# Optimization experiments

Hardware: AMD Instinct MI355X
Metric: run time of the kernel (lower is better)

The kernel has to match this reference:

```python
import jax, jax.numpy as jnp
import numpy as np
from jax.ops import segment_sum, segment_max

DIM = 64; EDGE_DIM = 6; ACTION_DIM = 6
N = 16384; E = 32768; G = 256; TPG = 12  # nodes, edges, graphs, torsions/graph


def setup_inputs() -> dict:
    key = jax.random.key(0)
    ks = jax.random.split(key, 16)
    d = DIM
    def lin(k, fo, fi):
        return (jax.random.normal(k, (fo, fi), jnp.float32) / np.sqrt(fi)).astype(jnp.float32)
    return {
        "x": jax.random.normal(ks[0], (N, 3), jnp.float32),
        "edge_attr": jax.random.normal(ks[1], (E, EDGE_DIM), jnp.float32),
        "edge_index": jax.random.randint(ks[2], (2, E), 0, N),
        "batch": (jnp.arange(N) // (N // G)).astype(jnp.int32),
        "nonring": jax.random.randint(ks[3], (G * TPG, 4), 0, N),
        "nrbidx": (jnp.arange(G * TPG) // TPG).astype(jnp.int32),
        "num_graphs": G,
        "torsion_size": TPG,
        "lin0_w": lin(ks[4], d, 3), "lin0_b": jnp.zeros((d,), jnp.float32),
        "e1_w": lin(ks[5], d, EDGE_DIM), "e1_b": jnp.zeros((d,), jnp.float32),
        "e2_w": lin(ks[6], d * d, d), "e2_b": jnp.zeros((d * d,), jnp.float32),
        "root_w": lin(ks[7], d, d), "conv_b": jnp.zeros((d,), jnp.float32),
        "gru_wih": lin(ks[8], 3 * d, d), "gru_whh": lin(ks[9], 3 * d, d),
        "gru_bih": jnp.zeros((3 * d,), jnp.float32), "gru_bhh": jnp.zeros((3 * d,), jnp.float32),
        "s2s_wih": lin(ks[10], 4 * d, 2 * d), "s2s_whh": lin(ks[11], 4 * d, d),
        "s2s_bih": jnp.zeros((4 * d,), jnp.float32), "s2s_bhh": jnp.zeros((4 * d,), jnp.float32),
        "mem_wih": lin(ks[12], 4 * d, 2 * d), "mem_whh": lin(ks[13], 4 * d, d),
        "mem_bih": jnp.zeros((4 * d,), jnp.float32), "mem_bhh": jnp.zeros((4 * d,), jnp.float32),
        "lin1_w": lin(ks[14], d, 5 * d), "lin1_b": jnp.zeros((d,), jnp.float32),
        "lin2_w": lin(ks[15], ACTION_DIM, d), "lin2_b": jnp.zeros((ACTION_DIM,), jnp.float32),
    }


def _lstm_step(xin, h, c, wih, whh, bih, bhh):
    g = xin @ wih.T + bih + h @ whh.T + bhh
    i, f, gg, o = jnp.split(g, 4, axis=-1)
    c = jax.nn.sigmoid(f) * c + jax.nn.sigmoid(i) * jnp.tanh(gg)
    h = jax.nn.sigmoid(o) * jnp.tanh(c)
    return h, c


def _model(x, edge_attr, lin0_w, lin0_b, e1_w, e1_b, e2_w, e2_b, root_w, conv_b,
           gru_wih, gru_whh, gru_bih, gru_bhh, s2s_wih, s2s_whh, s2s_bih, s2s_bhh,
           mem_wih, mem_whh, mem_bih, mem_bhh, lin1_w, lin1_b, lin2_w, lin2_b,
           edge_index, batch, nonring, nrbidx, num_graphs, torsion_size):
    d = lin0_w.shape[0]
    n = x.shape[0]
    out = jax.nn.relu(x @ lin0_w.T + lin0_b)           # [N, d]
    h = out                                            # GRU hidden
    src, dst = edge_index[0], edge_index[1]
    # edge-conditioned weights (fixed across the 6 iterations -> computed once)
    ew = (jax.nn.relu(edge_attr @ e1_w.T + e1_b) @ e2_w.T + e2_b).reshape(-1, d, d)  # [E, d, d]
    deg = jnp.clip(segment_sum(jnp.ones((src.shape[0],), out.dtype), dst, num_segments=n), 1.0)
    for _ in range(6):
        msg = jnp.einsum('ei,eio->eo', out[src], ew)   # per-edge matmul, [E, d]
        agg = segment_sum(msg, dst, num_segments=n) / deg[:, None]  # scatter-mean
        m = jax.nn.relu(agg + out @ root_w + conv_b)
        gi = m @ gru_wih.T + gru_bih
        gh = h @ gru_whh.T + gru_bhh
        r = jax.nn.sigmoid(gi[:, :d] + gh[:, :d])
        z = jax.nn.sigmoid(gi[:, d:2 * d] + gh[:, d:2 * d])
        nnew = jnp.tanh(gi[:, 2 * d:] + r * gh[:, 2 * d:])
        h = (1.0 - z) * nnew + z * h
        out = h
    # Set2Set pooling, 6 processing steps
    q_star = jnp.zeros((num_graphs, 2 * d), out.dtype)
    hs = jnp.zeros((num_graphs, d), out.dtype); cs = jnp.zeros_like(hs)
    for _ in range(6):
        hs, cs = _lstm_step(q_star, hs, cs, s2s_wih, s2s_whh, s2s_bih, s2s_bhh)
        e = jnp.sum(out * hs[batch], axis=-1)
        emax = segment_max(e, batch, num_segments=num_graphs)
        a = jnp.exp(e - emax[batch])
        a = a / segment_sum(a, batch, num_segments=num_graphs)[batch]
        r_ = segment_sum(a[:, None] * out, batch, num_segments=num_graphs)
        q_star = jnp.concatenate([hs, r_], axis=-1)
    # memory LSTM, single step from zero state
    hx = jnp.zeros((num_graphs, d), out.dtype); cx = jnp.zeros_like(hx)
    hx, cx = _lstm_step(q_star, hx, cx, mem_wih, mem_whh, mem_bih, mem_bhh)
    lstm_sel = hx[nrbidx]                                   # [T, d]
    node_sel = out[nonring.reshape(-1)].reshape(4, -1, d)   # faithful to .view(4,-1,dim)
    stacked = jnp.concatenate([lstm_sel[None], node_sel], axis=0)  # [5, T, d]
    feat = jnp.transpose(stacked, (2, 1, 0)).reshape(-1, 5 * d)    # faithful permute+reshape -> [T, 5d]
    o1 = jax.nn.relu(feat @ lin1_w.T + lin1_b)
    logits = o1 @ lin2_w.T + lin2_b                          # [T, action_dim]
    logit = logits.reshape(num_graphs, torsion_size, -1)     # uniform split + pad_sequence
    return logit, hx[None], cx[None]


def reference(x, edge_attr, edge_index, batch, nonring, nrbidx, num_graphs, torsion_size,
              lin0_w, lin0_b, e1_w, e1_b, e2_w, e2_b, root_w, conv_b,
              gru_wih, gru_whh, gru_bih, gru_bhh, s2s_wih, s2s_whh, s2s_bih, s2s_bhh,
              mem_wih, mem_whh, mem_bih, mem_bhh, lin1_w, lin1_b, lin2_w, lin2_b):
    return _model(x, edge_attr, lin0_w, lin0_b, e1_w, e1_b, e2_w, e2_b, root_w, conv_b,
                  gru_wih, gru_whh, gru_bih, gru_bhh, s2s_wih, s2s_whh, s2s_bih, s2s_bhh,
                  mem_wih, mem_whh, mem_bih, mem_bhh, lin1_w, lin1_b, lin2_w, lin2_b,
                  edge_index, batch, nonring, nrbidx, num_graphs, torsion_size)
```

## Files before the change

### kernel.cpp

```cpp
#include <hip/hip_runtime.h>

#define NNODE 16384
#define NEDGE 32768
#define NG    256
#define TPGx  12
#define TTOT  (NG * TPGx)
#define D     64

typedef _Float16 h8 __attribute__((ext_vector_type(8)));
typedef _Float16 h4 __attribute__((ext_vector_type(4)));
typedef float    f4 __attribute__((ext_vector_type(4)));

static __device__ __forceinline__ float sigm(float x) { return 1.f / (1.f + __expf(-x)); }
static __device__ __forceinline__ float tanh_f(float x) {
  float t = __expf(2.f * x);
  return (t - 1.f) / (t + 1.f);
}

static __device__ __forceinline__ f4 mfma16h(h8 a, h8 b, f4 c) {
  return __builtin_amdgcn_mfma_f32_16x16x32_f16(a, b, c, 0, 0, 0);
}

static __device__ __forceinline__ h8 splat16(_Float16 x) {
  h8 v = {x, x, x, x, x, x, x, x};
  return v;
}

#define WS_H      0
#define WS_AGG    4194304
#define WS_W2     8388608
#define WS_RT     8921088
#define WS_WHH    8929280
#define WS_WIH    8953856
#define WS_SWIHT  8978432
#define WS_SWHHT  9109504
#define WS_MWIHT  9175040
#define WS_L1WT   9306112
#define WS_L2WF   9388032
#define WS_FB     9389568
#define WS_DEG    9398784
#define WS_HX     9464320
#define WS_NEED   9529856

struct Srcs { const void* p[23]; };

__device__ __constant__ const int kCum[24] = {
    0, 192, 256, 640, 704, 262848, 266944, 271040, 271104, 283392, 295680,
    295872, 296064, 328832, 345216, 345472, 345728, 378496, 378752, 379008,
    399488, 399552, 399936, 399942};

__global__ __launch_bounds__(256) void setup1_kernel(Srcs S, char* __restrict__ ws) {
  int idx = blockIdx.x * 256 + threadIdx.x;
  if (idx < 399942) {
    int r = 0, base = 0;
#pragma unroll
    for (int k = 0; k < 23; k++)
      if (idx >= kCum[k]) { r = k; base = kCum[k]; }
    int li = idx - base;
    float v = ((const float*)S.p[r])[li];

    float*    fb    = (float*)(ws + WS_FB);
    _Float16* w2    = (_Float16*)(ws + WS_W2);
    _Float16* rtH   = (_Float16*)(ws + WS_RT);
    _Float16* whhH  = (_Float16*)(ws + WS_WHH);
    _Float16* wihH  = (_Float16*)(ws + WS_WIH);
    float*    swihT = (float*)(ws + WS_SWIHT);
    float*    swhhT = (float*)(ws + WS_SWHHT);
    float*    mwihT = (float*)(ws + WS_MWIHT);
    float*    l1wT  = (float*)(ws + WS_L1WT);
    float*    l2w   = (float*)(ws + WS_L2WF);

    switch (r) {
      case 0: fb[li] = v; break;
      case 1: fb[192 + li] = v; break;
      case 2: fb[256 + li] = v; break;
      case 3: fb[640 + li] = v; break;
      case 4: {
        int i = li >> 12, o = (li >> 6) & 63, k = li & 63;
        w2[i * 4096 + (((k >> 3) * 64 + o) << 3) + (k & 7)] = (_Float16)v;
      } break;
      case 5: {
        int k = li >> 6, o = li & 63;
        w2[64 * 4096 + (((k >> 3) * 64 + o) << 3) + (k & 7)] = (_Float16)v;
      } break;
      case 6: {
        int i = li >> 6, o = li & 63;
        rtH[o * 64 + i] = (_Float16)v;
      } break;
      case 7: fb[704 + li] = v; break;
      case 8: wihH[li] = (_Float16)v; break;
      case 9: whhH[li] = (_Float16)v; break;
      case 10: fb[768 + li] = v; break;
      case 11: fb[960 + li] = v; break;
      case 12: swihT[(li & 127) * 256 + (li >> 7)] = v; break;
      case 13: swhhT[(li & 63) * 256 + (li >> 6)] = v; break;
      case 14: fb[1152 + li] = v; break;
      case 15: fb[1408 + li] = v; break;
      case 16: mwihT[(li & 127) * 256 + (li >> 7)] = v; break;
      case 17: fb[1664 + li] = v; break;
      case 18: fb[1920 + li] = v; break;
      case 19: l1wT[(li % 320) * 64 + (li / 320)] = v; break;
      case 20: fb[2176 + li] = v; break;
      case 21: l2w[li] = v; break;
      case 22: fb[2240 + li] = v; break;
    }
    return;
  }
  idx -= 399942;
  float4 z4 = {0.f, 0.f, 0.f, 0.f};
  if (idx < 262144) { ((float4*)(ws + WS_AGG))[idx] = z4; return; }
  idx -= 262144;
  if (idx < 4096) ((float4*)(ws + WS_DEG))[idx] = z4;
}
#define SETUP1_N (399942 + 262144 + 4096)

__global__ __launch_bounds__(256) void setup2_kernel(
    const float* __restrict__ x, const int* __restrict__ edge_index,
    char* __restrict__ ws) {
  int idx = blockIdx.x * 256 + threadIdx.x;
  if (idx < 262144) {
    const float* fb = (const float*)(ws + WS_FB);
    float* h = (float*)(ws + WS_H);
    int n = idx >> 4, oq = idx & 15;
    float x0 = x[n * 3], x1 = x[n * 3 + 1], x2 = x[n * 3 + 2];
    float4 out;
#pragma unroll
    for (int c = 0; c < 4; c++) {
      int o = oq * 4 + c;
      float acc = fb[192 + o] + x0 * fb[o * 3] + x1 * fb[o * 3 + 1] + x2 * fb[o * 3 + 2];
      ((float*)&out)[c] = fmaxf(acc, 0.f);
    }
    *(float4*)&h[n * 64 + oq * 4] = out;
    return;
  }
  idx -= 262144;
  if (idx < NEDGE) {
    float* deg = (float*)(ws + WS_DEG);
    atomicAdd(&deg[edge_index[NEDGE + idx]], 1.0f);
  }
}
#define SETUP2_N (262144 + NEDGE)

__global__ __launch_bounds__(256) void msg_kernel(
    const float* __restrict__ h, const float* __restrict__ ea,
    const float* __restrict__ fb, const _Float16* __restrict__ w2,
    const int* __restrict__ edge_index, float* __restrict__ agg) {
  __shared__ _Float16 sOut[64][72];
  const int tid = threadIdx.x;
  const int wave = tid >> 6, lane = tid & 63;
  const int m15 = lane & 15, quad = lane >> 4;
  const int eb = blockIdx.x * 64;
  {
    int r = tid >> 2, c0 = (tid & 3) * 16;
    int srcn = edge_index[eb + r];
#pragma unroll
    for (int c = c0; c < c0 + 16; c += 4) {
      float4 v = *(const float4*)&h[srcn * D + c];
      sOut[r][c]     = (_Float16)v.x;
      sOut[r][c + 1] = (_Float16)v.y;
      sOut[r][c + 2] = (_Float16)v.z;
      sOut[r][c + 3] = (_Float16)v.w;
    }
  }
  h8 hid0[4], hid1[4];
#pragma unroll
  for (int r = 0; r < 4; r++) {
    int e = eb + r * 16 + m15;
    float eav[6];
#pragma unroll
    for (int j = 0; j < 6; j++) eav[j] = ea[e * 6 + j];
#pragma unroll
    for (int j = 0; j < 8; j++) {
      int k0 = quad * 8 + j, k1 = 32 + quad * 8 + j;
      float a0 = fb[640 + k0], a1 = fb[640 + k1];
#pragma unroll
      for (int jj = 0; jj < 6; jj++) {
        a0 += eav[jj] * fb[256 + k0 * 6 + jj];
        a1 += eav[jj] * fb[256 + k1 * 6 + jj];
      }
      hid0[r][j] = (_Float16)fmaxf(a0, 0.f);
      hid1[r][j] = (_Float16)fmaxf(a1, 0.f);
    }
  }
  __syncthreads();
  const _Float16* bp0 = w2 + (quad * 64 + wave * 16 + m15) * 8;
  const _Float16* bp1 = w2 + ((4 + quad) * 64 + wave * 16 + m15) * 8;
  f4 zz = {0.f, 0.f, 0.f, 0.f};
  f4 acc[4];
#pragma unroll
  for (int r = 0; r < 4; r++) acc[r] = zz;
  h8 c0[4], c1[4];
#pragma unroll
  for (int t = 0; t < 4; t++) {
    c0[t] = *(const h8*)(bp0 + t * 4096);
    c1[t] = *(const h8*)(bp1 + t * 4096);
  }
#pragma unroll
  for (int p = 0; p < 16; p++) {
    h8 n0[4], n1[4];
    if (p < 15) {
#pragma unroll
      for (int t = 0; t < 4; t++) {
        int i = (p + 1) * 4 + t;
        n0[t] = *(const h8*)(bp0 + i * 4096);
        n1[t] = *(const h8*)(bp1 + i * 4096);
      }
    }
#pragma unroll
    for (int r = 0; r < 4; r++) {
      h4 os4 = *(const h4*)&sOut[r * 16 + m15][p * 4];
#pragma unroll
      for (int t = 0; t < 4; t++) {
        h8 os = splat16(os4[t]);
        acc[r] = mfma16h(hid0[r] * os, c0[t], acc[r]);
        acc[r] = mfma16h(hid1[r] * os, c1[t], acc[r]);
      }
    }
    if (p < 15) {
#pragma unroll
      for (int t = 0; t < 4; t++) { c0[t] = n0[t]; c1[t] = n1[t]; }
    }
  }
  {
    h8 b0 = *(const h8*)(bp0 + 64 * 4096);
    h8 b1 = *(const h8*)(bp1 + 64 * 4096);
#pragma unroll
    for (int r = 0; r < 4; r++) {
      h8 a0 = *(const h8*)&sOut[r * 16 + m15][quad * 8];
      h8 a1 = *(const h8*)&sOut[r * 16 + m15][32 + quad * 8];
      acc[r] = mfma16h(a0, b0, acc[r]);
      acc[r] = mfma16h(a1, b1, acc[r]);
    }
  }
#pragma unroll
  for (int r = 0; r < 4; r++) {
#pragma unroll
    for (int reg = 0; reg < 4; reg++) {
      int ee = eb + r * 16 + quad * 4 + reg;
      int dn = edge_index[NEDGE + ee];
      atomicAdd(agg + dn * D + wave * 16 + m15, acc[r][reg]);
    }
  }
}

__global__ __launch_bounds__(64) void update_kernel(
    float* __restrict__ h, float* __restrict__ agg, const float* __restrict__ deg,
    const _Float16* __restrict__ rtH, const _Float16* __restrict__ whhH,
    const _Float16* __restrict__ wihH, const float* __restrict__ fb) {
  __shared__ float bufH[16][68];
  __shared__ float bufM[16][68];
  const int lane = threadIdx.x;
  const int m15 = lane & 15, quad = lane >> 4;
  const int nb = blockIdx.x * 16;
  {
    int r = lane >> 2, c0 = (lane & 3) * 16;
#pragma unroll
    for (int c = c0; c < c0 + 16; c += 4)
      *(float4*)&bufH[r][c] = *(const float4*)&h[(nb + r) * D + c];
  }
  __syncthreads();
  h8 a0, a1;
#pragma unroll
  for (int j = 0; j < 8; j++) {
    a0[j] = (_Float16)bufH[m15][quad * 8 + j];
    a1[j] = (_Float16)bufH[m15][32 + quad * 8 + j];
  }
  f4 zz = {0.f, 0.f, 0.f, 0.f};
  f4 acc[16];
#pragma unroll
  for (int nt = 0; nt < 16; nt++) acc[nt] = zz;
#pragma unroll
  for (int nt = 0; nt < 16; nt++) {
    int nn = nt * 16 + m15;
    const _Float16* bp = (nt < 4) ? (rtH + nn * D) : (whhH + (nn - 64) * D);
    h8 bh0 = *(const h8*)(bp + quad * 8);
    h8 bh1 = *(const h8*)(bp + 32 + quad * 8);
    f4 a = acc[nt];
    a = mfma16h(a0, bh0, a);
    a = mfma16h(a1, bh1, a);
    acc[nt] = a;
  }
#pragma unroll
  for (int nt = 0; nt < 4; nt++) {
#pragma unroll
    for (int reg = 0; reg < 4; reg++) {
      int nloc = quad * 4 + reg;
      int o = nt * 16 + m15;
      float dg = fmaxf(deg[nb + nloc], 1.f);
      int aidx = (nb + nloc) * D + o;
      float v = acc[nt][reg] + agg[aidx] / dg + fb[704 + o];
      agg[aidx] = 0.f;
      bufM[nloc][o] = fmaxf(v, 0.f);
    }
  }
  __syncthreads();
  h8 m0, m1;
#pragma unroll
  for (int j = 0; j < 8; j++) {
    m0[j] = (_Float16)bufM[m15][quad * 8 + j];
    m1[j] = (_Float16)bufM[m15][32 + quad * 8 + j];
  }
  f4 g2[12];
#pragma unroll
  for (int nt = 0; nt < 12; nt++) g2[nt] = zz;
#pragma unroll
  for (int nt = 0; nt < 12; nt++) {
    int nn = nt * 16 + m15;
    const _Float16* bp = wihH + nn * D;
    h8 bh0 = *(const h8*)(bp + quad * 8);
    h8 bh1 = *(const h8*)(bp + 32 + quad * 8);
    f4 a = g2[nt];
    a = mfma16h(m0, bh0, a);
    a = mfma16h(m1, bh1, a);
    g2[nt] = a;
  }
#pragma unroll
  for (int nt = 0; nt < 4; nt++) {
#pragma unroll
    for (int reg = 0; reg < 4; reg++) {
      int nloc = quad * 4 + reg;
      int o = nt * 16 + m15;
      int gidx = (nb + nloc) * D + o;
      float gir = g2[nt][reg]      + fb[768 + o];
      float giz = g2[nt + 4][reg]  + fb[768 + 64 + o];
      float gin = g2[nt + 8][reg]  + fb[768 + 128 + o];
      float ghr = acc[nt + 4][reg]  + fb[960 + o];
      float ghz = acc[nt + 8][reg]  + fb[960 + 64 + o];
      float ghn = acc[nt + 12][reg] + fb[960 + 128 + o];
      float rr = sigm(gir + ghr);
      float zg = sigm(giz + ghz);
      float nnv = tanh_f(gin + rr * ghn);
      float hv = h[gidx];
      h[gidx] = (1.f - zg) * nnv + zg * hv;
    }
  }
}

__global__ __launch_bounds__(256) void s2s_kernel(
    const float* __restrict__ h,
    const float* __restrict__ wihT, const float* __restrict__ whhT,
    const float* __restrict__ mwihT, const float* __restrict__ fb,
    float* __restrict__ hx_f32, float* __restrict__ dout) {
  __shared__ float outL[64][65];
  __shared__ float qs[128];
  __shared__ float hsv[64], csv[64], sg[256], sa[64];
  const int t = threadIdx.x;
  const int g = blockIdx.x;
  float wr[128];
#pragma unroll
  for (int j = 0; j < 128; j++) wr[j] = wihT[j * 256 + t];
  for (int idx = t; idx < 64 * 64; idx += 256) outL[idx >> 6][idx & 63] = h[g * 4096 + idx];
  if (t < 128) qs[t] = 0.f;
  if (t < 64) { hsv[t] = 0.f; csv[t] = 0.f; }
  __syncthreads();
  for (int step = 0; step < 6; step++) {
    float acc = fb[1152 + t] + fb[1408 + t];
#pragma unroll
    for (int j = 0; j < 128; j++) acc += qs[j] * wr[j];
#pragma unroll 8
    for (int j = 0; j < 64; j++) acc += hsv[j] * whhT[j * 256 + t];
    sg[t] = acc;
    __syncthreads();
    if (t < 64) {
      float cn = sigm(sg[64 + t]) * csv[t] + sigm(sg[t]) * tanh_f(sg[128 + t]);
      csv[t] = cn;
      float hv = sigm(sg[192 + t]) * tanh_f(cn);
      hsv[t] = hv;
      float e = 0.f;
      for (int d2 = 0; d2 < 64; d2++) e += outL[t][d2] * hsv[d2];
      float mx = e;
      for (int off = 32; off > 0; off >>= 1) mx = fmaxf(mx, __shfl_xor(mx, off));
      float a = __expf(e - mx);
      float s = a;
      for (int off = 32; off > 0; off >>= 1) s += __shfl_xor(s, off);
      sa[t] = a / s;
      float r = 0.f;
      for (int n2 = 0; n2 < 64; n2++) r += sa[n2] * outL[n2][t];
      qs[t] = hv;
      qs[64 + t] = r;
    }
    __syncthreads();
  }
  float acc = fb[1664 + t] + fb[1920 + t];
#pragma unroll 8
  for (int j = 0; j < 128; j++) acc += qs[j] * mwihT[j * 256 + t];
  sg[t] = acc;
  __syncthreads();
  if (t < 64) {
    float cn = sigm(sg[t]) * tanh_f(sg[128 + t]);
    float hn = sigm(sg[192 + t]) * tanh_f(cn);
    hx_f32[g * 64 + t] = hn;
    dout[TTOT * 6 + g * 64 + t] = hn;
    dout[TTOT * 6 + NG * 64 + g * 64 + t] = cn;
  }
}

__global__ __launch_bounds__(64) void head_kernel(
    const float* __restrict__ h, const float* __restrict__ hx_f32,
    const int* __restrict__ nonring, const int* __restrict__ nrbidx,
    const float* __restrict__ l1wT, const float* __restrict__ l2w,
    const float* __restrict__ fb, float* __restrict__ dout) {
  __shared__ float feat[320];
  __shared__ float so1[64];
  const int r = blockIdx.x;
  const int lane = threadIdx.x;
  const int blk = r % 48, di = r / 48;
  const int tt = blk * 64 + lane;
  feat[lane * 5] = hx_f32[nrbidx[tt] * 64 + di];
#pragma unroll
  for (int s = 1; s <= 4; s++)
    feat[lane * 5 + s] = h[nonring[(s - 1) * TTOT + tt] * 64 + di];
  __syncthreads();
  float acc = fb[2176 + lane];
#pragma unroll 8
  for (int c = 0; c < 320; c++) acc += feat[c] * l1wT[c * 64 + lane];
  so1[lane] = fmaxf(acc, 0.f);
  __syncthreads();
  if (lane < 6) {
    float a2 = fb[2240 + lane];
    for (int j = 0; j < 64; j++) a2 += so1[j] * l2w[lane * 64 + j];
    dout[r * 6 + lane] = a2;
  }
}

extern "C" void kernel_launch(void* const* d_in, const int* in_sizes, int n_in,
                              void* d_out, int out_size, void* d_ws, size_t ws_size,
                              hipStream_t stream) {
  (void)in_sizes; (void)n_in; (void)out_size;
  const float* x         = (const float*)d_in[0];
  const float* edge_attr = (const float*)d_in[1];
  const int* edge_index  = (const int*)d_in[2];
  const int* nonring     = (const int*)d_in[4];
  const int* nrbidx      = (const int*)d_in[5];
  float* out = (float*)d_out;

  char* ws = (char*)d_ws;
  float*    h      = (float*)(ws + WS_H);
  float*    agg    = (float*)(ws + WS_AGG);
  _Float16* w2     = (_Float16*)(ws + WS_W2);
  _Float16* rtH    = (_Float16*)(ws + WS_RT);
  _Float16* whhH   = (_Float16*)(ws + WS_WHH);
  _Float16* wihH   = (_Float16*)(ws + WS_WIH);
  float*    swihT  = (float*)(ws + WS_SWIHT);
  float*    swhhT  = (float*)(ws + WS_SWHHT);
  float*    mwihT  = (float*)(ws + WS_MWIHT);
  float*    l1wT   = (float*)(ws + WS_L1WT);
  float*    l2wF   = (float*)(ws + WS_L2WF);
  float*    fb     = (float*)(ws + WS_FB);
  float*    deg    = (float*)(ws + WS_DEG);
  float*    hx_f32 = (float*)(ws + WS_HX);
  if (ws_size < (size_t)WS_NEED) return;

  Srcs S;
  S.p[0] = d_in[8];   S.p[1] = d_in[9];   S.p[2] = d_in[10];  S.p[3] = d_in[11];
  S.p[4] = d_in[12];  S.p[5] = d_in[13];  S.p[6] = d_in[14];  S.p[7] = d_in[15];
  S.p[8] = d_in[16];  S.p[9] = d_in[17];  S.p[10] = d_in[18]; S.p[11] = d_in[19];
  S.p[12] = d_in[20]; S.p[13] = d_in[21]; S.p[14] = d_in[22]; S.p[15] = d_in[23];
  S.p[16] = d_in[24]; S.p[17] = d_in[26]; S.p[18] = d_in[27]; S.p[19] = d_in[28];
  S.p[20] = d_in[29]; S.p[21] = d_in[30]; S.p[22] = d_in[31];

  setup1_kernel<<<(SETUP1_N + 255) / 256, 256, 0, stream>>>(S, ws);
  setup2_kernel<<<(SETUP2_N + 255) / 256, 256, 0, stream>>>(x, edge_index, ws);

  for (int it = 0; it < 6; it++) {
    msg_kernel<<<NEDGE / 64, 256, 0, stream>>>(h, edge_attr, fb, w2, edge_index, agg);
    update_kernel<<<NNODE / 16, 64, 0, stream>>>(h, agg, deg, rtH, whhH, wihH, fb);
  }

  s2s_kernel<<<NG, 256, 0, stream>>>(h, swihT, swhhT, mwihT, fb, hx_f32, out);
  head_kernel<<<TTOT, 64, 0, stream>>>(h, hx_f32, nonring, nrbidx, l1wT, l2wF, fb, out);
}
```

Measured before the change: 444.5 us.

## Replace atomic scatter aggregation with CSR gather of per-edge messages

Edge messages are now written to a dense per-edge buffer, and a CSR index of incoming edges per destination node is built once at setup. The update kernel sums each node's messages by gathering through that index, so the float atomics and the per-iteration zeroing of the aggregation buffer go away. Update blocks now handle 8 nodes instead of 16, which doubles the grid but leaves half of each MFMA tile idle. The cost is an extra 8 MB message buffer write and read per iteration, plus two small setup kernels, one of which is a single-block serial prefix scan.

```diff
diff --git a/kernel.cpp b/kernel.cpp
--- a/kernel.cpp
+++ b/kernel.cpp
@@ -27,20 +27,23 @@
 }
 
 #define WS_H      0
-#define WS_AGG    4194304
-#define WS_W2     8388608
-#define WS_RT     8921088
-#define WS_WHH    8929280
-#define WS_WIH    8953856
-#define WS_SWIHT  8978432
-#define WS_SWHHT  9109504
-#define WS_MWIHT  9175040
-#define WS_L1WT   9306112
-#define WS_L2WF   9388032
-#define WS_FB     9389568
-#define WS_DEG    9398784
-#define WS_HX     9464320
-#define WS_NEED   9529856
+#define WS_MSG    4194304
+#define WS_W2     12582912
+#define WS_RT     13115392
+#define WS_WHH    13123584
+#define WS_WIH    13148160
+#define WS_SWIHT  13172736
+#define WS_SWHHT  13303808
+#define WS_MWIHT  13369344
+#define WS_L1WT   13500416
+#define WS_L2WF   13582336
+#define WS_FB     13583872
+#define WS_DEG    13592896
+#define WS_CSROFF 13658432
+#define WS_CURS   13723984
+#define WS_CSRE   13789520
+#define WS_HX     13920592
+#define WS_NEED   13986304
 
 struct Srcs { const void* p[23]; };
 
@@ -108,11 +111,9 @@
   }
   idx -= 399942;
   float4 z4 = {0.f, 0.f, 0.f, 0.f};
-  if (idx < 262144) { ((float4*)(ws + WS_AGG))[idx] = z4; return; }
-  idx -= 262144;
   if (idx < 4096) ((float4*)(ws + WS_DEG))[idx] = z4;
 }
-#define SETUP1_N (399942 + 262144 + 4096)
+#define SETUP1_N (399942 + 4096)
 
 __global__ __launch_bounds__(256) void setup2_kernel(
     const float* __restrict__ x, const int* __restrict__ edge_index,
@@ -141,10 +142,47 @@
 }
 #define SETUP2_N (262144 + NEDGE)
 
+__global__ __launch_bounds__(256) void setup3_kernel(char* __restrict__ ws) {
+  __shared__ int part[256];
+  const float* deg = (const float*)(ws + WS_DEG);
+  int* csroff = (int*)(ws + WS_CSROFF);
+  int* curs   = (int*)(ws + WS_CURS);
+  const int t = threadIdx.x;
+  int s = 0;
+  for (int j = 0; j < 64; j++) s += (int)deg[t * 64 + j];
+  part[t] = s;
+  __syncthreads();
+  if (t == 0) {
+    int run = 0;
+    for (int k = 0; k < 256; k++) { int v = part[k]; part[k] = run; run += v; }
+  }
+  __syncthreads();
+  int off = part[t];
+  for (int j = 0; j < 64; j++) {
+    int n = t * 64 + j;
+    csroff[n] = off;
+    off += (int)deg[n];
+    curs[n] = 0;
+  }
+  if (t == 255) csroff[NNODE] = NEDGE;
+}
+
+__global__ __launch_bounds__(256) void setup4_kernel(const int* __restrict__ edge_index,
+                                                     char* __restrict__ ws) {
+  int e = blockIdx.x * 256 + threadIdx.x;
+  if (e >= NEDGE) return;
+  const int* csroff = (const int*)(ws + WS_CSROFF);
+  int* curs = (int*)(ws + WS_CURS);
+  int* csre = (int*)(ws + WS_CSRE);
+  int dst = edge_index[NEDGE + e];
+  int pos = atomicAdd(&curs[dst], 1);
+  csre[csroff[dst] + pos] = e;
+}
+
 __global__ __launch_bounds__(256) void msg_kernel(
     const float* __restrict__ h, const float* __restrict__ ea,
     const float* __restrict__ fb, const _Float16* __restrict__ w2,
-    const int* __restrict__ edge_index, float* __restrict__ agg) {
+    const int* __restrict__ edge_index, float* __restrict__ msgbuf) {
   __shared__ _Float16 sOut[64][72];
   const int tid = threadIdx.x;
   const int wave = tid >> 6, lane = tid & 63;
@@ -237,33 +275,53 @@
 #pragma unroll
     for (int reg = 0; reg < 4; reg++) {
       int ee = eb + r * 16 + quad * 4 + reg;
-      int dn = edge_index[NEDGE + ee];
-      atomicAdd(agg + dn * D + wave * 16 + m15, acc[r][reg]);
+      msgbuf[ee * D + wave * 16 + m15] = acc[r][reg];
     }
   }
 }
 
 __global__ __launch_bounds__(64) void update_kernel(
-    float* __restrict__ h, float* __restrict__ agg, const float* __restrict__ deg,
+    float* __restrict__ h, const float* __restrict__ msgbuf,
+    const float* __restrict__ deg, const int* __restrict__ csroff,
+    const int* __restrict__ csre,
     const _Float16* __restrict__ rtH, const _Float16* __restrict__ whhH,
     const _Float16* __restrict__ wihH, const float* __restrict__ fb) {
-  __shared__ float bufH[16][68];
-  __shared__ float bufM[16][68];
+  __shared__ float bufH[8][68];
+  __shared__ float bufM[8][68];
   const int lane = threadIdx.x;
   const int m15 = lane & 15, quad = lane >> 4;
-  const int nb = blockIdx.x * 16;
+  const int m7 = m15 & 7;
+  const int nb = blockIdx.x * 8;
   {
-    int r = lane >> 2, c0 = (lane & 3) * 16;
-#pragma unroll
-    for (int c = c0; c < c0 + 16; c += 4)
+    int r = lane >> 3, c0 = (lane & 7) * 8;
+#pragma unroll
+    for (int c = c0; c < c0 + 8; c += 4)
       *(float4*)&bufH[r][c] = *(const float4*)&h[(nb + r) * D + c];
   }
   __syncthreads();
+  float aggv[4][4];
+#pragma unroll
+  for (int reg = 0; reg < 4; reg++)
+#pragma unroll
+    for (int nt = 0; nt < 4; nt++) aggv[reg][nt] = 0.f;
+#pragma unroll
+  for (int reg = 0; reg < 4; reg++) {
+    int nloc = quad * 4 + reg;
+    if (nloc < 8) {
+      int n = nb + nloc;
+      int be = csroff[n], en = csroff[n + 1];
+      for (int e2 = be; e2 < en; e2++) {
+        const float* mp = msgbuf + csre[e2] * D + m15;
+#pragma unroll
+        for (int nt = 0; nt < 4; nt++) aggv[reg][nt] += mp[nt * 16];
+      }
+    }
+  }
   h8 a0, a1;
 #pragma unroll
   for (int j = 0; j < 8; j++) {
-    a0[j] = (_Float16)bufH[m15][quad * 8 + j];
-    a1[j] = (_Float16)bufH[m15][32 + quad * 8 + j];
+    a0[j] = (_Float16)bufH[m7][quad * 8 + j];
+    a1[j] = (_Float16)bufH[m7][32 + quad * 8 + j];
   }
   f4 zz = {0.f, 0.f, 0.f, 0.f};
   f4 acc[16];
@@ -285,20 +343,20 @@
 #pragma unroll
     for (int reg = 0; reg < 4; reg++) {
       int nloc = quad * 4 + reg;
-      int o = nt * 16 + m15;
-      float dg = fmaxf(deg[nb + nloc], 1.f);
-      int aidx = (nb + nloc) * D + o;
-      float v = acc[nt][reg] + agg[aidx] / dg + fb[704 + o];
-      agg[aidx] = 0.f;
-      bufM[nloc][o] = fmaxf(v, 0.f);
+      if (nloc < 8) {
+        int o = nt * 16 + m15;
+        float dg = fmaxf(deg[nb + nloc], 1.f);
+        float v = acc[nt][reg] + aggv[reg][nt] / dg + fb[704 + o];
+        bufM[nloc][o] = fmaxf(v, 0.f);
+      }
     }
   }
   __syncthreads();
   h8 m0, m1;
 #pragma unroll
   for (int j = 0; j < 8; j++) {
-    m0[j] = (_Float16)bufM[m15][quad * 8 + j];
-    m1[j] = (_Float16)bufM[m15][32 + quad * 8 + j];
+    m0[j] = (_Float16)bufM[m7][quad * 8 + j];
+    m1[j] = (_Float16)bufM[m7][32 + quad * 8 + j];
   }
   f4 g2[12];
 #pragma unroll
@@ -319,19 +377,21 @@
 #pragma unroll
     for (int reg = 0; reg < 4; reg++) {
       int nloc = quad * 4 + reg;
-      int o = nt * 16 + m15;
-      int gidx = (nb + nloc) * D + o;
-      float gir = g2[nt][reg]      + fb[768 + o];
-      float giz = g2[nt + 4][reg]  + fb[768 + 64 + o];
-      float gin = g2[nt + 8][reg]  + fb[768 + 128 + o];
-      float ghr = acc[nt + 4][reg]  + fb[960 + o];
-      float ghz = acc[nt + 8][reg]  + fb[960 + 64 + o];
-      float ghn = acc[nt + 12][reg] + fb[960 + 128 + o];
-      float rr = sigm(gir + ghr);
-      float zg = sigm(giz + ghz);
-      float nnv = tanh_f(gin + rr * ghn);
-      float hv = h[gidx];
-      h[gidx] = (1.f - zg) * nnv + zg * hv;
+      if (nloc < 8) {
+        int o = nt * 16 + m15;
+        int gidx = (nb + nloc) * D + o;
+        float gir = g2[nt][reg]      + fb[768 + o];
+        float giz = g2[nt + 4][reg]  + fb[768 + 64 + o];
+        float gin = g2[nt + 8][reg]  + fb[768 + 128 + o];
+        float ghr = acc[nt + 4][reg]  + fb[960 + o];
+        float ghz = acc[nt + 8][reg]  + fb[960 + 64 + o];
+        float ghn = acc[nt + 12][reg] + fb[960 + 128 + o];
+        float rr = sigm(gir + ghr);
+        float zg = sigm(giz + ghz);
+        float nnv = tanh_f(gin + rr * ghn);
+        float hv = h[gidx];
+        h[gidx] = (1.f - zg) * nnv + zg * hv;
+      }
     }
   }
 }
@@ -436,7 +496,7 @@
 
   char* ws = (char*)d_ws;
   float*    h      = (float*)(ws + WS_H);
-  float*    agg    = (float*)(ws + WS_AGG);
+  float*    msgbuf = (float*)(ws + WS_MSG);
   _Float16* w2     = (_Float16*)(ws + WS_W2);
   _Float16* rtH    = (_Float16*)(ws + WS_RT);
   _Float16* whhH   = (_Float16*)(ws + WS_WHH);
@@ -448,6 +508,8 @@
   float*    l2wF   = (float*)(ws + WS_L2WF);
   float*    fb     = (float*)(ws + WS_FB);
   float*    deg    = (float*)(ws + WS_DEG);
+  int*      csroff = (int*)(ws + WS_CSROFF);
+  int*      csre   = (int*)(ws + WS_CSRE);
   float*    hx_f32 = (float*)(ws + WS_HX);
   if (ws_size < (size_t)WS_NEED) return;
 
@@ -461,10 +523,13 @@
 
   setup1_kernel<<<(SETUP1_N + 255) / 256, 256, 0, stream>>>(S, ws);
   setup2_kernel<<<(SETUP2_N + 255) / 256, 256, 0, stream>>>(x, edge_index, ws);
+  setup3_kernel<<<1, 256, 0, stream>>>(ws);
+  setup4_kernel<<<NEDGE / 256, 256, 0, stream>>>(edge_index, ws);
 
   for (int it = 0; it < 6; it++) {
-    msg_kernel<<<NEDGE / 64, 256, 0, stream>>>(h, edge_attr, fb, w2, edge_index, agg);
-    update_kernel<<<NNODE / 16, 64, 0, stream>>>(h, agg, deg, rtH, whhH, wihH, fb);
+    msg_kernel<<<NEDGE / 64, 256, 0, stream>>>(h, edge_attr, fb, w2, edge_index, msgbuf);
+    update_kernel<<<NNODE / 8, 64, 0, stream>>>(h, msgbuf, deg, csroff, csre,
+                                                rtH, whhH, wihH, fb);
   }
 
   s2s_kernel<<<NG, 256, 0, stream>>>(h, swihT, swhhT, mwihT, fb, hx_f32, out);
```

Result: slower. 513.0 us (+15.4%).

## Split message kernel K-dimension across two wave halves with shared-memory reduction

Applied to the files above, without the earlier changes.

The message kernel now launches 512 threads per block, with two groups of four waves each handling half of the 64 input-feature chunks of the edge-conditioned weight product. The second half adds the root term and writes its partial accumulators to shared memory. After a barrier the first half sums the partials and performs the atomic scatter. This halves the serial MFMA chain per wave to raise parallelism and latency hiding, at the cost of extra LDS use, a second barrier and duplicated edge-hidden computation in each half.

```diff
diff --git a/kernel.cpp b/kernel.cpp
--- a/kernel.cpp
+++ b/kernel.cpp
@@ -141,20 +141,23 @@
 }
 #define SETUP2_N (262144 + NEDGE)
 
-__global__ __launch_bounds__(256) void msg_kernel(
+__global__ __launch_bounds__(512, 4) void msg_kernel(
     const float* __restrict__ h, const float* __restrict__ ea,
     const float* __restrict__ fb, const _Float16* __restrict__ w2,
     const int* __restrict__ edge_index, float* __restrict__ agg) {
   __shared__ _Float16 sOut[64][72];
+  __shared__ float part[4][64][17];
   const int tid = threadIdx.x;
   const int wave = tid >> 6, lane = tid & 63;
   const int m15 = lane & 15, quad = lane >> 4;
+  const int w4 = wave & 3;
+  const int half = wave >> 2;
   const int eb = blockIdx.x * 64;
   {
-    int r = tid >> 2, c0 = (tid & 3) * 16;
+    int r = tid >> 3, c0 = (tid & 7) * 8;
     int srcn = edge_index[eb + r];
 #pragma unroll
-    for (int c = c0; c < c0 + 16; c += 4) {
+    for (int c = c0; c < c0 + 8; c += 4) {
       float4 v = *(const float4*)&h[srcn * D + c];
       sOut[r][c]     = (_Float16)v.x;
       sOut[r][c + 1] = (_Float16)v.y;
@@ -183,62 +186,74 @@
     }
   }
   __syncthreads();
-  const _Float16* bp0 = w2 + (quad * 64 + wave * 16 + m15) * 8;
-  const _Float16* bp1 = w2 + ((4 + quad) * 64 + wave * 16 + m15) * 8;
+  const _Float16* bp0 = w2 + (quad * 64 + w4 * 16 + m15) * 8;
+  const _Float16* bp1 = w2 + ((4 + quad) * 64 + w4 * 16 + m15) * 8;
+  const int tbase = half * 32;
   f4 zz = {0.f, 0.f, 0.f, 0.f};
   f4 acc[4];
 #pragma unroll
   for (int r = 0; r < 4; r++) acc[r] = zz;
-  h8 c0[4], c1[4];
+  h8 c0v[4], c1v[4];
 #pragma unroll
   for (int t = 0; t < 4; t++) {
-    c0[t] = *(const h8*)(bp0 + t * 4096);
-    c1[t] = *(const h8*)(bp1 + t * 4096);
-  }
-#pragma unroll
-  for (int p = 0; p < 16; p++) {
+    c0v[t] = *(const h8*)(bp0 + (tbase + t) * 4096);
+    c1v[t] = *(const h8*)(bp1 + (tbase + t) * 4096);
+  }
+#pragma unroll
+  for (int p = 0; p < 8; p++) {
     h8 n0[4], n1[4];
-    if (p < 15) {
+    if (p < 7) {
 #pragma unroll
       for (int t = 0; t < 4; t++) {
-        int i = (p + 1) * 4 + t;
+        int i = tbase + (p + 1) * 4 + t;
         n0[t] = *(const h8*)(bp0 + i * 4096);
         n1[t] = *(const h8*)(bp1 + i * 4096);
       }
     }
 #pragma unroll
     for (int r = 0; r < 4; r++) {
-      h4 os4 = *(const h4*)&sOut[r * 16 + m15][p * 4];
+      h4 os4 = *(const h4*)&sOut[r * 16 + m15][tbase + p * 4];
 #pragma unroll
       for (int t = 0; t < 4; t++) {
         h8 os = splat16(os4[t]);
-        acc[r] = mfma16h(hid0[r] * os, c0[t], acc[r]);
-        acc[r] = mfma16h(hid1[r] * os, c1[t], acc[r]);
+        acc[r] = mfma16h(hid0[r] * os, c0v[t], acc[r]);
+        acc[r] = mfma16h(hid1[r] * os, c1v[t], acc[r]);
       }
     }
-    if (p < 15) {
-#pragma unroll
-      for (int t = 0; t < 4; t++) { c0[t] = n0[t]; c1[t] = n1[t]; }
-    }
-  }
-  {
-    h8 b0 = *(const h8*)(bp0 + 64 * 4096);
-    h8 b1 = *(const h8*)(bp1 + 64 * 4096);
+    if (p < 7) {
+#pragma unroll
+      for (int t = 0; t < 4; t++) { c0v[t] = n0[t]; c1v[t] = n1[t]; }
+    }
+  }
+  if (half == 1) {
+    {
+      h8 b0 = *(const h8*)(bp0 + 64 * 4096);
+      h8 b1 = *(const h8*)(bp1 + 64 * 4096);
+#pragma unroll
+      for (int r = 0; r < 4; r++) {
+        h8 a0 = *(const h8*)&sOut[r * 16 + m15][quad * 8];
+        h8 a1 = *(const h8*)&sOut[r * 16 + m15][32 + quad * 8];
+        acc[r] = mfma16h(a0, b0, acc[r]);
+        acc[r] = mfma16h(a1, b1, acc[r]);
+      }
+    }
+#pragma unroll
+    for (int r = 0; r < 4; r++)
+#pragma unroll
+      for (int reg = 0; reg < 4; reg++)
+        part[w4][r * 16 + quad * 4 + reg][m15] = acc[r][reg];
+  }
+  __syncthreads();
+  if (half == 0) {
 #pragma unroll
     for (int r = 0; r < 4; r++) {
-      h8 a0 = *(const h8*)&sOut[r * 16 + m15][quad * 8];
-      h8 a1 = *(const h8*)&sOut[r * 16 + m15][32 + quad * 8];
-      acc[r] = mfma16h(a0, b0, acc[r]);
-      acc[r] = mfma16h(a1, b1, acc[r]);
-    }
-  }
-#pragma unroll
-  for (int r = 0; r < 4; r++) {
-#pragma unroll
-    for (int reg = 0; reg < 4; reg++) {
-      int ee = eb + r * 16 + quad * 4 + reg;
-      int dn = edge_index[NEDGE + ee];
-      atomicAdd(agg + dn * D + wave * 16 + m15, acc[r][reg]);
+#pragma unroll
+      for (int reg = 0; reg < 4; reg++) {
+        int el = r * 16 + quad * 4 + reg;
+        float v = acc[r][reg] + part[w4][el][m15];
+        int dn = edge_index[NEDGE + eb + el];
+        atomicAdd(agg + dn * D + w4 * 16 + m15, v);
+      }
     }
   }
 }
@@ -463,7 +478,7 @@
   setup2_kernel<<<(SETUP2_N + 255) / 256, 256, 0, stream>>>(x, edge_index, ws);
 
   for (int it = 0; it < 6; it++) {
-    msg_kernel<<<NEDGE / 64, 256, 0, stream>>>(h, edge_attr, fb, w2, edge_index, agg);
+    msg_kernel<<<NEDGE / 64, 512, 0, stream>>>(h, edge_attr, fb, w2, edge_index, agg);
     update_kernel<<<NNODE / 16, 64, 0, stream>>>(h, agg, deg, rtH, whhH, wihH, fb);
   }
 
```

Result: slower. 1.045 ms (+135.0%).
